# Performance work log

Hardware: AMD Instinct MI355X
Metric: run time of the kernel (lower is better)

Reference implementation:

```python
import jax, jax.numpy as jnp
import numpy as np
from jax import lax

EPS = 1e-5  # BatchNorm eps (inference-style BN with running stats)


def _bn(x, g, b, m, v):
    scale = g / jnp.sqrt(v + EPS)
    return x * scale[None, :, None, None] + (b - m * scale)[None, :, None, None]


def _conv1x1_bn(x, w, g, b, m, v):
    # ConvNormActivation(in_ch, out, k=1, activation=None) -> 1x1 conv (no bias) + BN
    y = jnp.einsum('bchw,oc->bohw', x, w)
    return _bn(y, g, b, m, v)


def _upsample_bilinear_ac(x, scale):
    # nn.Upsample(scale_factor=scale, mode='bilinear', align_corners=True)
    B, C, H, W = x.shape
    Ho, Wo = H * scale, W * scale

    def coords(n_in, n_out):
        s = jnp.arange(n_out, dtype=x.dtype) * ((n_in - 1) / (n_out - 1))
        i0 = jnp.clip(jnp.floor(s).astype(jnp.int32), 0, n_in - 2)
        t = s - i0.astype(x.dtype)
        return i0, t

    iy, ty = coords(H, Ho)
    ix, tx = coords(W, Wo)
    x = x[:, :, iy, :] * (1 - ty)[None, None, :, None] + x[:, :, iy + 1, :] * ty[None, None, :, None]
    x = x[:, :, :, ix] * (1 - tx) + x[:, :, :, ix + 1] * tx
    return x


def _dcnv2(x, off_w, off_b, w):
    # DCNv2: internal 3x3 conv -> 18 offsets (dy,dx per tap) + 9 sigmoid masks,
    # then modulated deformable 3x3 conv (stride 1, pad 1, no bias).
    B, C, H, W = x.shape
    K2 = 9
    om = lax.conv_general_dilated(x, off_w, (1, 1), ((1, 1), (1, 1)),
                                  dimension_numbers=('NCHW', 'OIHW', 'NCHW'))
    om = om + off_b[None, :, None, None]
    off = om[:, :2 * K2].reshape(B, K2, 2, H, W)          # (dy, dx) per kernel tap
    mask = jax.nn.sigmoid(om[:, 2 * K2:3 * K2])           # [B,9,H,W]

    ky, kx = jnp.meshgrid(jnp.arange(3), jnp.arange(3), indexing='ij')
    base_y = (jnp.arange(H)[None, :, None] + (ky.reshape(K2) - 1)[:, None, None]).astype(x.dtype)  # [9,H,1]
    base_x = (jnp.arange(W)[None, None, :] + (kx.reshape(K2) - 1)[:, None, None]).astype(x.dtype)  # [9,1,W]
    sy = base_y[None] + off[:, :, 0]                      # [B,9,H,W]
    sx = base_x[None] + off[:, :, 1]

    xf = x.reshape(B, C, H * W)
    y0 = jnp.floor(sy)
    x0 = jnp.floor(sx)
    val = jnp.zeros((B, C, K2, H, W), x.dtype)
    for dy in (0, 1):
        for dx in (0, 1):
            yy = y0 + dy
            xx = x0 + dx
            wgt = (1 - jnp.abs(sy - yy)) * (1 - jnp.abs(sx - xx))
            valid = (yy >= 0) & (yy <= H - 1) & (xx >= 0) & (xx <= W - 1)
            idx = jnp.clip(yy, 0, H - 1).astype(jnp.int32) * W + jnp.clip(xx, 0, W - 1).astype(jnp.int32)
            g = jnp.take_along_axis(xf, idx.reshape(B, 1, -1), axis=2).reshape(B, C, K2, H, W)
            val = val + g * (wgt * valid.astype(x.dtype))[:, None]
    val = val * mask[:, None]
    return jnp.einsum('bckhw,ock->bohw', val, w.reshape(w.shape[0], C, K2))


def _forward(f0, f1, f2, f3,
             w0, g0, b0, m0, v0, w1, g1, b1, m1, v1,
             w2, g2, b2, m2, v2, w3, g3, b3, m3, v3,
             off_w, off_b, dcn_w, gf, bf, mf, vf):
    x1 = _conv1x1_bn(f0, w0, g0, b0, m0, v0)
    x2 = _upsample_bilinear_ac(_conv1x1_bn(f1, w1, g1, b1, m1, v1), 2)
    x3 = _upsample_bilinear_ac(_conv1x1_bn(f2, w2, g2, b2, m2, v2), 4)
    x4 = _upsample_bilinear_ac(_conv1x1_bn(f3, w3, g3, b3, m3, v3), 8)
    x = jax.nn.relu(x1 + x2 + x3 + x4)
    y = _dcnv2(x, off_w, off_b, dcn_w)
    return jax.nn.relu(_bn(y, gf, bf, mf, vf))


def setup_inputs() -> dict:
    key = jax.random.key(0)
    ks = iter(jax.random.split(key, 64))

    def rn(shape, scale=1.0):
        return jax.random.normal(next(ks), shape, dtype=jnp.float32) * scale

    def ru(shape):
        return jax.random.uniform(next(ks), shape, dtype=jnp.float32)

    C = 64
    inp = {}
    inp['f0'] = rn((4, 64, 160, 160))
    inp['f1'] = rn((4, 128, 80, 80))
    inp['f2'] = rn((4, 256, 40, 40))
    inp['f3'] = rn((4, 512, 20, 20))
    for i, cin in enumerate([64, 128, 256, 512]):
        inp[f'w{i}'] = rn((C, cin), 1.0 / np.sqrt(cin))
        inp[f'g{i}'] = rn((C,))
        inp[f'b{i}'] = rn((C,))
        inp[f'm{i}'] = rn((C,))
        inp[f'v{i}'] = ru((C,))
    inp['off_w'] = rn((27, C, 3, 3), 0.01)   # small offsets, like post-training DCN
    inp['off_b'] = rn((27,), 0.01)
    inp['dcn_w'] = rn((C, C, 3, 3), 1.0 / np.sqrt(C * 9))
    inp['gf'] = rn((C,))
    inp['bf'] = rn((C,))
    inp['mf'] = rn((C,))
    inp['vf'] = ru((C,))
    return inp


def reference(f0, f1, f2, f3,
              w0, g0, b0, m0, v0, w1, g1, b1, m1, v1,
              w2, g2, b2, m2, v2, w3, g3, b3, m3, v3,
              off_w, off_b, dcn_w, gf, bf, mf, vf):
    return _forward(f0, f1, f2, f3,
                    w0, g0, b0, m0, v0, w1, g1, b1, m1, v1,
                    w2, g2, b2, m2, v2, w3, g3, b3, m3, v3,
                    off_w, off_b, dcn_w, gf, bf, mf, vf)
```

## Files before the change

kernel.cpp:

```cpp
#include <hip/hip_runtime.h>
#include <math.h>

#define EPSB 1e-5f

constexpr int B_ = 4;
constexpr int C_ = 64;
constexpr int H_ = 160;
constexpr int W_ = 160;
constexpr int HW_ = H_ * W_;

constexpr size_t X_OFF   = 0;
constexpr size_t Y1_OFF  = X_OFF  + (size_t)B_ * HW_ * 64;
constexpr size_t Y2_OFF  = Y1_OFF + (size_t)B_ * 6400 * 64;
constexpr size_t Y3_OFF  = Y2_OFF + (size_t)B_ * 1600 * 64;
constexpr size_t OM_OFF  = Y3_OFF + (size_t)B_ * 400 * 64;
constexpr size_t WR0_OFF = OM_OFF + (size_t)B_ * HW_ * 27;
constexpr size_t WTB_OFF = WR0_OFF + 4096;
constexpr size_t RWB_OFF = WTB_OFF + (9 * 64 * 72) / 2;
constexpr size_t SB_OFF  = RWB_OFF + (9 * 32 * 64) / 2;
constexpr size_t WR1_OFF = X_OFF + 0;
constexpr size_t WR2_OFF = X_OFF + 8192;
constexpr size_t WR3_OFF = X_OFF + 24576;

typedef short bf16x8 __attribute__((ext_vector_type(8)));
typedef float f32x4 __attribute__((ext_vector_type(4)));
typedef unsigned int u32x2 __attribute__((ext_vector_type(2)));

static __device__ __forceinline__ unsigned short f2bf(float f) {
    unsigned int u = __float_as_uint(f);
    u += 0x7fff + ((u >> 16) & 1);
    return (unsigned short)(u >> 16);
}

__global__ __launch_bounds__(256) void prep_kernel(
    const float* __restrict__ g0, const float* __restrict__ b0, const float* __restrict__ m0, const float* __restrict__ v0,
    const float* __restrict__ g1, const float* __restrict__ b1, const float* __restrict__ m1, const float* __restrict__ v1,
    const float* __restrict__ g2, const float* __restrict__ b2, const float* __restrict__ m2, const float* __restrict__ v2,
    const float* __restrict__ g3, const float* __restrict__ b3, const float* __restrict__ m3, const float* __restrict__ v3,
    const float* __restrict__ gf, const float* __restrict__ bf, const float* __restrict__ mf, const float* __restrict__ vf,
    const float* __restrict__ w0, const float* __restrict__ w1, const float* __restrict__ w2, const float* __restrict__ w3,
    const float* __restrict__ dcn_w, const float* __restrict__ off_w,
    float* __restrict__ ws)
{
    int tid = blockIdx.x * 256 + threadIdx.x;
    if (tid < 320) {
        int j = tid >> 6, c = tid & 63;
        const float *g, *b, *m, *v;
        switch (j) {
            case 0: g = g0; b = b0; m = m0; v = v0; break;
            case 1: g = g1; b = b1; m = m1; v = v1; break;
            case 2: g = g2; b = b2; m = m2; v = v2; break;
            case 3: g = g3; b = b3; m = m3; v = v3; break;
            default: g = gf; b = bf; m = mf; v = vf; break;
        }
        float sc = g[c] * rsqrtf(v[c] + EPSB);
        ws[SB_OFF + j * 128 + c]      = sc;
        ws[SB_OFF + j * 128 + 64 + c] = b[c] - m[c] * sc;
        return;
    }
    int t = tid - 320;
    if (t < 4096) {
        int ci = t >> 6, o = t & 63;
        ws[WR0_OFF + t] = w0[o * 64 + ci];
        return;
    }
    t -= 4096;
    if (t < 9 * 64 * 72) {
        int k = t / 4608, r = t % 4608, o = r / 72, c = r % 72;
        float v = (c < 64) ? dcn_w[o * 576 + c * 9 + k] : 0.f;
        ((unsigned short*)(ws + WTB_OFF))[t] = f2bf(v);
        return;
    }
    t -= 9 * 64 * 72;
    if (t < 9 * 32 * 64) {
        int tap = t >> 11, r = t & 2047, o = r >> 6, ci = r & 63;
        float v = (o < 27) ? off_w[o * 576 + ci * 9 + tap] : 0.f;
        ((unsigned short*)(ws + RWB_OFF))[t] = f2bf(v);
        return;
    }
    t -= 9 * 32 * 64;
    if (t < 8192) {
        int ci = t >> 6, o = t & 63;
        ws[WR1_OFF + t] = w1[o * 128 + ci];
        return;
    }
    t -= 8192;
    if (t < 16384) {
        int ci = t >> 6, o = t & 63;
        ws[WR2_OFF + t] = w2[o * 256 + ci];
        return;
    }
    t -= 16384;
    if (t < 32768) {
        int ci = t >> 6, o = t & 63;
        ws[WR3_OFF + t] = w3[o * 512 + ci];
        return;
    }
}

__global__ __launch_bounds__(256) void conv_all_kernel(
    const float* __restrict__ f1in, const float* __restrict__ f2in, const float* __restrict__ f3in,
    float* __restrict__ ws)
{
    __shared__ float R0[64 * 65];
    __shared__ float R1[64 * 65];
    __shared__ float SBl[128];

    int blk = blockIdx.x;
    const float* fin; const float* wr; const float* sbg; float* yout;
    int Cin, hw, tile;
    if (blk < 400)      { fin = f1in; wr = ws + WR1_OFF; sbg = ws + SB_OFF + 128; yout = ws + Y1_OFF; Cin = 128; hw = 6400; tile = blk; }
    else if (blk < 500) { fin = f2in; wr = ws + WR2_OFF; sbg = ws + SB_OFF + 256; yout = ws + Y2_OFF; Cin = 256; hw = 1600; tile = blk - 400; }
    else                { fin = f3in; wr = ws + WR3_OFF; sbg = ws + SB_OFF + 384; yout = ws + Y3_OFF; Cin = 512; hw = 400;  tile = blk - 500; }

    int tid  = threadIdx.x;
    int lane = tid & 63;
    int wv   = __builtin_amdgcn_readfirstlane(tid >> 6);

    if (tid < 128) SBl[tid] = sbg[tid];

    int P = tile * 64 + lane;
    int b = P / hw;
    int p = P - b * hw;

    int cq = Cin >> 2;
    const float* fb = fin + ((size_t)b * Cin + (size_t)wv * cq) * hw + p;
    const float* wq = wr + (wv * cq) * 64;

    float acc[64];
#pragma unroll
    for (int o = 0; o < 64; o++) acc[o] = 0.f;

    for (int c0 = 0; c0 < cq; c0 += 8) {
        float fv[8];
#pragma unroll
        for (int j = 0; j < 8; j++) fv[j] = fb[(size_t)(c0 + j) * hw];
#pragma unroll
        for (int j = 0; j < 8; j++) {
            const float* wrow = wq + (c0 + j) * 64;
#pragma unroll
            for (int o = 0; o < 64; o++) acc[o] = fmaf(fv[j], wrow[o], acc[o]);
        }
    }

    if (wv == 2) {
#pragma unroll
        for (int o = 0; o < 64; o++) R0[lane * 65 + o] = acc[o];
    }
    if (wv == 3) {
#pragma unroll
        for (int o = 0; o < 64; o++) R1[lane * 65 + o] = acc[o];
    }
    __syncthreads();
    if (wv == 0) {
#pragma unroll
        for (int o = 0; o < 64; o++) acc[o] += R0[lane * 65 + o];
    }
    if (wv == 1) {
#pragma unroll
        for (int o = 0; o < 64; o++) acc[o] += R1[lane * 65 + o];
    }
    __syncthreads();
    if (wv == 1) {
#pragma unroll
        for (int o = 0; o < 64; o++) R0[lane * 65 + o] = acc[o];
    }
    __syncthreads();
    if (wv == 0) {
#pragma unroll
        for (int o = 0; o < 64; o++) {
            float v = acc[o] + R0[lane * 65 + o];
            R1[lane * 65 + o] = fmaf(v, SBl[o], SBl[64 + o]);
        }
    }
    __syncthreads();

#pragma unroll
    for (int it = 0; it < 16; it++) {
        int idx = it * 256 + tid;
        int px = idx >> 6, o = idx & 63;
        yout[(size_t)(tile * 64 + px) * 64 + o] = R1[px * 65 + o];
    }
}

__global__ __launch_bounds__(256) void fuse_kernel(const float* __restrict__ f0, float* __restrict__ ws)
{
    __shared__ float Ot[64 * 68];

    int tid = threadIdx.x;
    int blk = blockIdx.x;
    int xcd = blk & 7, slot = blk >> 3;
    int b = xcd >> 1;
    int t = (xcd & 1) * 200 + slot;
    int p0 = t * 64;
    int lane = tid & 63;
    int cb = __builtin_amdgcn_readfirstlane(tid >> 6);
    int p = p0 + lane;
    const float* wr0 = ws + WR0_OFF + cb * 16;
    const float* sb  = ws + SB_OFF;

    {
        float acc[16];
#pragma unroll
        for (int i = 0; i < 16; i++) acc[i] = 0.f;

        const float* f0b = f0 + (size_t)b * 64 * HW_ + p;
        for (int ci0 = 0; ci0 < 64; ci0 += 16) {
            float fv[16];
#pragma unroll
            for (int j = 0; j < 16; j++) fv[j] = f0b[(size_t)(ci0 + j) * HW_];
#pragma unroll
            for (int j = 0; j < 16; j++) {
                const float* wrow = wr0 + (ci0 + j) * 64;
#pragma unroll
                for (int i = 0; i < 16; i++) acc[i] = fmaf(fv[j], wrow[i], acc[i]);
            }
        }
        float* orow = Ot + lane * 68 + cb * 16;
#pragma unroll
        for (int i = 0; i < 16; i++) {
            int o = cb * 16 + i;
            orow[i] = fmaf(acc[i], sb[o], sb[64 + o]);
        }
    }
    __syncthreads();

    {
        int chunk = lane & 15, pxo = lane >> 4;
        unsigned short* xb = (unsigned short*)(ws + X_OFF) + ((size_t)b * HW_ + p0) * 64;
#pragma unroll
        for (int r = 0; r < 4; r++) {
            int gpx = cb * 16 + r * 4 + pxo;
            int gp = p0 + gpx;
            int h = gp / W_, w = gp % W_;

            float fy1 = h * (79.f / 159.f); int i1 = (int)fy1; if (i1 > 78) i1 = 78; float ty1 = fy1 - i1;
            float fx1 = w * (79.f / 159.f); int j1 = (int)fx1; if (j1 > 78) j1 = 78; float tx1 = fx1 - j1;
            const float* y1 = ws + Y1_OFF + ((size_t)b * 6400 + (size_t)(i1 * 80 + j1)) * 64 + chunk * 4;
            float fy2 = h * (39.f / 159.f); int i2 = (int)fy2; if (i2 > 38) i2 = 38; float ty2 = fy2 - i2;
            float fx2 = w * (39.f / 159.f); int j2 = (int)fx2; if (j2 > 38) j2 = 38; float tx2 = fx2 - j2;
            const float* y2 = ws + Y2_OFF + ((size_t)b * 1600 + (size_t)(i2 * 40 + j2)) * 64 + chunk * 4;
            float fy3 = h * (19.f / 159.f); int i3 = (int)fy3; if (i3 > 18) i3 = 18; float ty3 = fy3 - i3;
            float fx3 = w * (19.f / 159.f); int j3 = (int)fx3; if (j3 > 18) j3 = 18; float tx3 = fx3 - j3;
            const float* y3 = ws + Y3_OFF + ((size_t)b * 400 + (size_t)(i3 * 20 + j3)) * 64 + chunk * 4;

            f32x4 A[12];
            A[0]  = *(const f32x4*)(y1);
            A[1]  = *(const f32x4*)(y1 + 64);
            A[2]  = *(const f32x4*)(y1 + 80 * 64);
            A[3]  = *(const f32x4*)(y1 + 81 * 64);
            A[4]  = *(const f32x4*)(y2);
            A[5]  = *(const f32x4*)(y2 + 64);
            A[6]  = *(const f32x4*)(y2 + 40 * 64);
            A[7]  = *(const f32x4*)(y2 + 41 * 64);
            A[8]  = *(const f32x4*)(y3);
            A[9]  = *(const f32x4*)(y3 + 64);
            A[10] = *(const f32x4*)(y3 + 20 * 64);
            A[11] = *(const f32x4*)(y3 + 21 * 64);

            f32x4 v = *(const f32x4*)(Ot + gpx * 68 + chunk * 4);

            float w00, w01, w10, w11;
            w00 = (1.f - ty1) * (1.f - tx1); w01 = (1.f - ty1) * tx1; w10 = ty1 * (1.f - tx1); w11 = ty1 * tx1;
#pragma unroll
            for (int j = 0; j < 4; j++)
                v[j] += A[0][j] * w00 + A[1][j] * w01 + A[2][j] * w10 + A[3][j] * w11;
            w00 = (1.f - ty2) * (1.f - tx2); w01 = (1.f - ty2) * tx2; w10 = ty2 * (1.f - tx2); w11 = ty2 * tx2;
#pragma unroll
            for (int j = 0; j < 4; j++)
                v[j] += A[4][j] * w00 + A[5][j] * w01 + A[6][j] * w10 + A[7][j] * w11;
            w00 = (1.f - ty3) * (1.f - tx3); w01 = (1.f - ty3) * tx3; w10 = ty3 * (1.f - tx3); w11 = ty3 * tx3;
#pragma unroll
            for (int j = 0; j < 4; j++)
                v[j] += A[8][j] * w00 + A[9][j] * w01 + A[10][j] * w10 + A[11][j] * w11;

#pragma unroll
            for (int j = 0; j < 4; j++) v[j] = fmaxf(v[j], 0.f);
            unsigned int lo = ((unsigned int)f2bf(v[1]) << 16) | f2bf(v[0]);
            unsigned int hi = ((unsigned int)f2bf(v[3]) << 16) | f2bf(v[2]);
            *(u32x2*)(xb + (size_t)gpx * 64 + chunk * 4) = (u32x2){lo, hi};
        }
    }
}

__global__ __launch_bounds__(256, 8) void dcn_fused_kernel(const float* __restrict__ off_b,
                                                           float* __restrict__ ws, float* __restrict__ out)
{
    __shared__ __align__(16) unsigned char SMEM[16640];
    unsigned short* A  = (unsigned short*)SMEM;
    float*          OMs = (float*)(SMEM + 9216);

    int tid = threadIdx.x;
    int blk = blockIdx.x;
    int xcd = blk & 7, slot = blk >> 3;
    int b = xcd >> 1;
    int t = (xcd & 1) * 200 + slot;
    int p0 = t * 64;
    int lane = tid & 63, cb = tid >> 6;
    int px = lane;
    int p = p0 + px;
    int h = p / W_, w = p % W_;
    int mrow = lane & 15, quad = lane >> 4;
    int chunk = lane & 15, pxo = lane >> 4;

    const unsigned short* rwb = (const unsigned short*)(ws + RWB_OFF);
    const unsigned short* wtb = (const unsigned short*)(ws + WTB_OFF);
    const unsigned short* xbh = (const unsigned short*)(ws + X_OFF) + (size_t)b * HW_ * 64;
    const float* sb = ws + SB_OFF + 4 * 128;

    {
        f32x4 acc2[2];
        acc2[0] = (f32x4){0.f, 0.f, 0.f, 0.f};
        acc2[1] = (f32x4){0.f, 0.f, 0.f, 0.f};

        for (int tap = 0; tap < 9; ++tap) {
            int dy = tap / 3 - 1, dx = tap % 3 - 1;
            int delta = dy * W_ + dx;
            int  pss[4];
            bool vlds[4];
#pragma unroll
            for (int r = 0; r < 4; r++) {
                int gpx = cb * 16 + r * 4 + pxo;
                int gp = p0 + gpx;
                int gh = gp / W_, gw = gp % W_;
                int yy = gh + dy, xx = gw + dx;
                vlds[r] = (yy >= 0) && (yy < H_) && (xx >= 0) && (xx < W_);
                int ps = gp + delta;
                pss[r] = min(max(ps, 0), HW_ - 1);
            }
            u32x2 g[4];
#pragma unroll
            for (int r = 0; r < 4; r++)
                g[r] = *(const u32x2*)(xbh + (size_t)pss[r] * 64 + chunk * 4);
#pragma unroll
            for (int r = 0; r < 4; r++) {
                int gpx = cb * 16 + r * 4 + pxo;
                u32x2 gv;
                gv.x = vlds[r] ? g[r].x : 0u;
                gv.y = vlds[r] ? g[r].y : 0u;
                *(u32x2*)(A + gpx * 72 + chunk * 4) = gv;
            }

            const unsigned short* Ab = A + (cb * 16 + mrow) * 72;
#pragma unroll
            for (int ks = 0; ks < 2; ks++) {
                bf16x8 af = *(const bf16x8*)(Ab + ks * 32 + quad * 8);
#pragma unroll
                for (int nt = 0; nt < 2; nt++) {
                    bf16x8 bf_ = *(const bf16x8*)(rwb + tap * 2048 + (nt * 16 + mrow) * 64 + ks * 32 + quad * 8);
                    acc2[nt] = __builtin_amdgcn_mfma_f32_16x16x32_bf16(af, bf_, acc2[nt], 0, 0, 0);
                }
            }
        }

        __syncthreads();
        float* Cl = (float*)SMEM;
#pragma unroll
        for (int nt = 0; nt < 2; nt++) {
            int o = nt * 16 + mrow;
            if (o < 27) {
                int pr = cb * 16 + quad * 4;
#pragma unroll
                for (int r = 0; r < 4; r++) Cl[(pr + r) * 28 + o] = acc2[nt][r];
            }
        }
        __syncthreads();

        for (int k = cb; k < 9; k += 4) {
            float ady = Cl[px * 28 + 2 * k]     + off_b[2 * k];
            float adx = Cl[px * 28 + 2 * k + 1] + off_b[2 * k + 1];
            float am  = Cl[px * 28 + 18 + k]    + off_b[18 + k];
            float sy = (float)(h + k / 3 - 1) + ady;
            float sx = (float)(w + k % 3 - 1) + adx;
            float mk = 1.f / (1.f + __expf(-am));
            OMs[px * 27 + 3 * k]     = sy;
            OMs[px * 27 + 3 * k + 1] = sx;
            OMs[px * 27 + 3 * k + 2] = mk;
        }
        __syncthreads();
    }

    f32x4 acc[4];
#pragma unroll
    for (int nt = 0; nt < 4; nt++) acc[nt] = (f32x4){0.f, 0.f, 0.f, 0.f};

    for (int k = 0; k < 9; ++k) {
#pragma unroll
        for (int rp = 0; rp < 2; rp++) {
            int   idxs[2][4];
            float wvs[2][4];
#pragma unroll
            for (int rr = 0; rr < 2; rr++) {
                int r = rp * 2 + rr;
                int gpx = cb * 16 + r * 4 + pxo;
                float sy = OMs[gpx * 27 + 3 * k];
                float sx = OMs[gpx * 27 + 3 * k + 1];
                float mk = OMs[gpx * 27 + 3 * k + 2];
                float y0f = floorf(sy), x0f = floorf(sx);
                int y0 = (int)y0f, x0 = (int)x0f;
                float ty = sy - y0f, tx = sx - x0f;
#pragma unroll
                for (int cr = 0; cr < 4; cr++) {
                    int dy = cr >> 1, dx = cr & 1;
                    int yy = y0 + dy, xx = x0 + dx;
                    float wy = dy ? ty : 1.f - ty;
                    float wx = dx ? tx : 1.f - tx;
                    bool vld = (yy >= 0) && (yy < H_) && (xx >= 0) && (xx < W_);
                    int yc = min(max(yy, 0), H_ - 1);
                    int xc = min(max(xx, 0), W_ - 1);
                    idxs[rr][cr] = yc * W_ + xc;
                    wvs[rr][cr]  = vld ? wy * wx * mk : 0.f;
                }
            }
            u32x2 g[2][4];
#pragma unroll
            for (int rr = 0; rr < 2; rr++)
#pragma unroll
                for (int cr = 0; cr < 4; cr++)
                    g[rr][cr] = *(const u32x2*)(xbh + (size_t)idxs[rr][cr] * 64 + chunk * 4);
#pragma unroll
            for (int rr = 0; rr < 2; rr++) {
                int r = rp * 2 + rr;
                int gpx = cb * 16 + r * 4 + pxo;
                f32x4 v = (f32x4){0.f, 0.f, 0.f, 0.f};
#pragma unroll
                for (int cr = 0; cr < 4; cr++) {
                    float wv = wvs[rr][cr];
                    float e0 = __uint_as_float(g[rr][cr].x << 16);
                    float e1 = __uint_as_float(g[rr][cr].x & 0xffff0000u);
                    float e2 = __uint_as_float(g[rr][cr].y << 16);
                    float e3 = __uint_as_float(g[rr][cr].y & 0xffff0000u);
                    v[0] = fmaf(e0, wv, v[0]);
                    v[1] = fmaf(e1, wv, v[1]);
                    v[2] = fmaf(e2, wv, v[2]);
                    v[3] = fmaf(e3, wv, v[3]);
                }
                unsigned int lo = ((unsigned int)f2bf(v[1]) << 16) | f2bf(v[0]);
                unsigned int hi = ((unsigned int)f2bf(v[3]) << 16) | f2bf(v[2]);
                *(u32x2*)(A + gpx * 72 + chunk * 4) = (u32x2){lo, hi};
            }
        }

        const unsigned short* Ab = A + (cb * 16 + mrow) * 72;
#pragma unroll
        for (int ks = 0; ks < 2; ks++) {
            bf16x8 af = *(const bf16x8*)(Ab + ks * 32 + quad * 8);
#pragma unroll
            for (int nt = 0; nt < 4; nt++) {
                bf16x8 bf_ = *(const bf16x8*)(wtb + k * 4608 + (nt * 16 + mrow) * 72 + ks * 32 + quad * 8);
                acc[nt] = __builtin_amdgcn_mfma_f32_16x16x32_bf16(af, bf_, acc[nt], 0, 0, 0);
            }
        }
    }

    __syncthreads();
    float* C_lds = (float*)SMEM;
#pragma unroll
    for (int nt = 0; nt < 4; nt++) {
        int o = nt * 16 + mrow;
        int pxb = cb * 16 + quad * 4;
#pragma unroll
        for (int r = 0; r < 4; r++) C_lds[o * 65 + pxb + r] = acc[nt][r];
    }
    __syncthreads();
#pragma unroll
    for (int i = 0; i < 16; i++) {
        int o = cb * 16 + i;
        float v = C_lds[o * 65 + lane];
        v = fmaf(v, sb[o], sb[64 + o]);
        out[((size_t)b * 64 + o) * HW_ + p0 + lane] = fmaxf(v, 0.f);
    }
}

extern "C" void kernel_launch(void* const* d_in, const int* in_sizes, int n_in,
                              void* d_out, int out_size, void* d_ws, size_t ws_size,
                              hipStream_t stream)
{
    const float* f0 = (const float*)d_in[0];
    const float* f1 = (const float*)d_in[1];
    const float* f2 = (const float*)d_in[2];
    const float* f3 = (const float*)d_in[3];
    const float* w0 = (const float*)d_in[4];
    const float* g0 = (const float*)d_in[5];
    const float* b0 = (const float*)d_in[6];
    const float* m0 = (const float*)d_in[7];
    const float* v0 = (const float*)d_in[8];
    const float* w1 = (const float*)d_in[9];
    const float* g1 = (const float*)d_in[10];
    const float* b1 = (const float*)d_in[11];
    const float* m1 = (const float*)d_in[12];
    const float* v1 = (const float*)d_in[13];
    const float* w2 = (const float*)d_in[14];
    const float* g2 = (const float*)d_in[15];
    const float* b2 = (const float*)d_in[16];
    const float* m2 = (const float*)d_in[17];
    const float* v2 = (const float*)d_in[18];
    const float* w3 = (const float*)d_in[19];
    const float* g3 = (const float*)d_in[20];
    const float* b3 = (const float*)d_in[21];
    const float* m3 = (const float*)d_in[22];
    const float* v3 = (const float*)d_in[23];
    const float* off_w = (const float*)d_in[24];
    const float* off_b = (const float*)d_in[25];
    const float* dcn_w = (const float*)d_in[26];
    const float* gf = (const float*)d_in[27];
    const float* bf = (const float*)d_in[28];
    const float* mf = (const float*)d_in[29];
    const float* vf = (const float*)d_in[30];

    float* ws  = (float*)d_ws;
    float* out = (float*)d_out;

    prep_kernel<<<dim3(476), dim3(256), 0, stream>>>(
        g0, b0, m0, v0, g1, b1, m1, v1, g2, b2, m2, v2, g3, b3, m3, v3,
        gf, bf, mf, vf, w0, w1, w2, w3, dcn_w, off_w, ws);

    conv_all_kernel<<<dim3(525), dim3(256), 0, stream>>>(f1, f2, f3, ws);

    fuse_kernel<<<dim3(1600), dim3(256), 0, stream>>>(f0, ws);

    dcn_fused_kernel<<<dim3(1600), dim3(256), 0, stream>>>(off_b, ws, out);
}
```

Measured before the change: 299.6 us.

## Merge low-res and f0 1x1 convs into one launch, split upsample-fuse out

The f0 1x1 conv+BN moves out of the fuse kernel into one combined launch with the f1/f2/f3 1x1 convs. Its result goes to a bf16 workspace buffer so the two kinds of work can share the GPU instead of running back to back. A new fuse2 kernel reads that buffer, adds the three bilinear-upsampled branches, applies ReLU and writes the bf16 input for the DCN. In exchange this adds a global round trip of the intermediate, rounds it to bf16 earlier, and the channel-split reduction now uses a single LDS buffer with extra barriers.

```diff
diff --git a/kernel.cpp b/kernel.cpp
--- a/kernel.cpp
+++ b/kernel.cpp
@@ -21,6 +21,8 @@
 constexpr size_t WR1_OFF = X_OFF + 0;
 constexpr size_t WR2_OFF = X_OFF + 8192;
 constexpr size_t WR3_OFF = X_OFF + 24576;
+constexpr size_t XU_X = 0;
+constexpr size_t XU_O = 6553600;
 
 typedef short bf16x8 __attribute__((ext_vector_type(8)));
 typedef float f32x4 __attribute__((ext_vector_type(4)));
@@ -30,6 +32,9 @@
     unsigned int u = __float_as_uint(f);
     u += 0x7fff + ((u >> 16) & 1);
     return (unsigned short)(u >> 16);
+}
+static __device__ __forceinline__ float bf2f(unsigned short s) {
+    return __uint_as_float((unsigned int)s << 16);
 }
 
 __global__ __launch_bounds__(256) void prep_kernel(
@@ -98,95 +103,140 @@
     }
 }
 
-__global__ __launch_bounds__(256) void conv_all_kernel(
-    const float* __restrict__ f1in, const float* __restrict__ f2in, const float* __restrict__ f3in,
+__global__ __launch_bounds__(256) void produce_kernel(
+    const float* __restrict__ f0in, const float* __restrict__ f1in,
+    const float* __restrict__ f2in, const float* __restrict__ f3in,
     float* __restrict__ ws)
 {
-    __shared__ float R0[64 * 65];
-    __shared__ float R1[64 * 65];
-    __shared__ float SBl[128];
+    __shared__ __align__(16) unsigned char SM[16640];
 
     int blk = blockIdx.x;
-    const float* fin; const float* wr; const float* sbg; float* yout;
-    int Cin, hw, tile;
-    if (blk < 400)      { fin = f1in; wr = ws + WR1_OFF; sbg = ws + SB_OFF + 128; yout = ws + Y1_OFF; Cin = 128; hw = 6400; tile = blk; }
-    else if (blk < 500) { fin = f2in; wr = ws + WR2_OFF; sbg = ws + SB_OFF + 256; yout = ws + Y2_OFF; Cin = 256; hw = 1600; tile = blk - 400; }
-    else                { fin = f3in; wr = ws + WR3_OFF; sbg = ws + SB_OFF + 384; yout = ws + Y3_OFF; Cin = 512; hw = 400;  tile = blk - 500; }
-
     int tid  = threadIdx.x;
     int lane = tid & 63;
-    int wv   = __builtin_amdgcn_readfirstlane(tid >> 6);
-
-    if (tid < 128) SBl[tid] = sbg[tid];
-
-    int P = tile * 64 + lane;
-    int b = P / hw;
-    int p = P - b * hw;
-
-    int cq = Cin >> 2;
-    const float* fb = fin + ((size_t)b * Cin + (size_t)wv * cq) * hw + p;
-    const float* wq = wr + (wv * cq) * 64;
-
-    float acc[64];
-#pragma unroll
-    for (int o = 0; o < 64; o++) acc[o] = 0.f;
-
-    for (int c0 = 0; c0 < cq; c0 += 8) {
-        float fv[8];
-#pragma unroll
-        for (int j = 0; j < 8; j++) fv[j] = fb[(size_t)(c0 + j) * hw];
-#pragma unroll
-        for (int j = 0; j < 8; j++) {
-            const float* wrow = wq + (c0 + j) * 64;
-#pragma unroll
-            for (int o = 0; o < 64; o++) acc[o] = fmaf(fv[j], wrow[o], acc[o]);
-        }
-    }
-
-    if (wv == 2) {
-#pragma unroll
-        for (int o = 0; o < 64; o++) R0[lane * 65 + o] = acc[o];
-    }
-    if (wv == 3) {
-#pragma unroll
-        for (int o = 0; o < 64; o++) R1[lane * 65 + o] = acc[o];
-    }
-    __syncthreads();
-    if (wv == 0) {
-#pragma unroll
-        for (int o = 0; o < 64; o++) acc[o] += R0[lane * 65 + o];
-    }
-    if (wv == 1) {
-#pragma unroll
-        for (int o = 0; o < 64; o++) acc[o] += R1[lane * 65 + o];
-    }
-    __syncthreads();
-    if (wv == 1) {
-#pragma unroll
-        for (int o = 0; o < 64; o++) R0[lane * 65 + o] = acc[o];
-    }
-    __syncthreads();
-    if (wv == 0) {
-#pragma unroll
-        for (int o = 0; o < 64; o++) {
-            float v = acc[o] + R0[lane * 65 + o];
-            R1[lane * 65 + o] = fmaf(v, SBl[o], SBl[64 + o]);
-        }
-    }
-    __syncthreads();
-
-#pragma unroll
-    for (int it = 0; it < 16; it++) {
-        int idx = it * 256 + tid;
-        int px = idx >> 6, o = idx & 63;
-        yout[(size_t)(tile * 64 + px) * 64 + o] = R1[px * 65 + o];
-    }
-}
-
-__global__ __launch_bounds__(256) void fuse_kernel(const float* __restrict__ f0, float* __restrict__ ws)
+
+    if (blk < 525) {
+        float* R0 = (float*)SM;
+        const float* fin; const float* wr; const float* sbg; float* yout;
+        int Cin, hw, tile;
+        if (blk < 400)      { fin = f1in; wr = ws + WR1_OFF; sbg = ws + SB_OFF + 128; yout = ws + Y1_OFF; Cin = 128; hw = 6400; tile = blk; }
+        else if (blk < 500) { fin = f2in; wr = ws + WR2_OFF; sbg = ws + SB_OFF + 256; yout = ws + Y2_OFF; Cin = 256; hw = 1600; tile = blk - 400; }
+        else                { fin = f3in; wr = ws + WR3_OFF; sbg = ws + SB_OFF + 384; yout = ws + Y3_OFF; Cin = 512; hw = 400;  tile = blk - 500; }
+
+        int wv = __builtin_amdgcn_readfirstlane(tid >> 6);
+
+        int P = tile * 64 + lane;
+        int b = P / hw;
+        int p = P - b * hw;
+
+        int cq = Cin >> 2;
+        const float* fb = fin + ((size_t)b * Cin + (size_t)wv * cq) * hw + p;
+        const float* wq = wr + (wv * cq) * 64;
+
+        float acc[64];
+#pragma unroll
+        for (int o = 0; o < 64; o++) acc[o] = 0.f;
+
+        for (int c0 = 0; c0 < cq; c0 += 8) {
+            float fv[8];
+#pragma unroll
+            for (int j = 0; j < 8; j++) fv[j] = fb[(size_t)(c0 + j) * hw];
+#pragma unroll
+            for (int j = 0; j < 8; j++) {
+                const float* wrow = wq + (c0 + j) * 64;
+#pragma unroll
+                for (int o = 0; o < 64; o++) acc[o] = fmaf(fv[j], wrow[o], acc[o]);
+            }
+        }
+
+        if (wv == 2) {
+#pragma unroll
+            for (int o = 0; o < 64; o++) R0[lane * 65 + o] = acc[o];
+        }
+        __syncthreads();
+        if (wv == 0) {
+#pragma unroll
+            for (int o = 0; o < 64; o++) acc[o] += R0[lane * 65 + o];
+        }
+        __syncthreads();
+        if (wv == 3) {
+#pragma unroll
+            for (int o = 0; o < 64; o++) R0[lane * 65 + o] = acc[o];
+        }
+        __syncthreads();
+        if (wv == 1) {
+#pragma unroll
+            for (int o = 0; o < 64; o++) acc[o] += R0[lane * 65 + o];
+        }
+        __syncthreads();
+        if (wv == 1) {
+#pragma unroll
+            for (int o = 0; o < 64; o++) R0[lane * 65 + o] = acc[o];
+        }
+        __syncthreads();
+        if (wv == 0) {
+#pragma unroll
+            for (int o = 0; o < 64; o++) {
+                float v = acc[o] + R0[lane * 65 + o];
+                R0[lane * 65 + o] = fmaf(v, sbg[o], sbg[64 + o]);
+            }
+        }
+        __syncthreads();
+
+#pragma unroll
+        for (int it = 0; it < 16; it++) {
+            int idx = it * 256 + tid;
+            int px = idx >> 6, o = idx & 63;
+            yout[(size_t)(tile * 64 + px) * 64 + o] = R0[px * 65 + o];
+        }
+    } else {
+        unsigned short* Ot = (unsigned short*)SM;
+        int fblk = blk - 525;
+        int xcd = fblk & 7, slot = fblk >> 3;
+        int b = xcd >> 1;
+        int t = (xcd & 1) * 200 + slot;
+        int p0 = t * 64;
+        int cb = __builtin_amdgcn_readfirstlane(tid >> 6);
+        int p = p0 + lane;
+        const float* wr0 = ws + WR0_OFF + cb * 16;
+        const float* sb  = ws + SB_OFF;
+
+        float acc[16];
+#pragma unroll
+        for (int i = 0; i < 16; i++) acc[i] = 0.f;
+
+        const float* f0b = f0in + (size_t)b * 64 * HW_ + p;
+        for (int ci0 = 0; ci0 < 64; ci0 += 8) {
+            float fv[8];
+#pragma unroll
+            for (int j = 0; j < 8; j++) fv[j] = f0b[(size_t)(ci0 + j) * HW_];
+#pragma unroll
+            for (int j = 0; j < 8; j++) {
+                const float* wrow = wr0 + (ci0 + j) * 64;
+#pragma unroll
+                for (int i = 0; i < 16; i++) acc[i] = fmaf(fv[j], wrow[i], acc[i]);
+            }
+        }
+        unsigned short* orow = Ot + lane * 68 + cb * 16;
+#pragma unroll
+        for (int i = 0; i < 16; i++) {
+            int o = cb * 16 + i;
+            orow[i] = f2bf(fmaf(acc[i], sb[o], sb[64 + o]));
+        }
+        __syncthreads();
+
+        unsigned short* Ob = (unsigned short*)ws + XU_O + ((size_t)b * HW_ + p0) * 64;
+#pragma unroll
+        for (int it = 0; it < 8; it++) {
+            int idx = it * 256 + tid;
+            int px = idx >> 5, seg = idx & 31;
+            *(unsigned int*)(Ob + (size_t)px * 64 + seg * 2) =
+                *(const unsigned int*)(Ot + px * 68 + seg * 2);
+        }
+    }
+}
+
+__global__ __launch_bounds__(256) void fuse2_kernel(float* __restrict__ ws)
 {
-    __shared__ float Ot[64 * 68];
-
     int tid = threadIdx.x;
     int blk = blockIdx.x;
     int xcd = blk & 7, slot = blk >> 3;
@@ -195,91 +245,67 @@
     int p0 = t * 64;
     int lane = tid & 63;
     int cb = __builtin_amdgcn_readfirstlane(tid >> 6);
-    int p = p0 + lane;
-    const float* wr0 = ws + WR0_OFF + cb * 16;
-    const float* sb  = ws + SB_OFF;
-
-    {
-        float acc[16];
-#pragma unroll
-        for (int i = 0; i < 16; i++) acc[i] = 0.f;
-
-        const float* f0b = f0 + (size_t)b * 64 * HW_ + p;
-        for (int ci0 = 0; ci0 < 64; ci0 += 16) {
-            float fv[16];
-#pragma unroll
-            for (int j = 0; j < 16; j++) fv[j] = f0b[(size_t)(ci0 + j) * HW_];
-#pragma unroll
-            for (int j = 0; j < 16; j++) {
-                const float* wrow = wr0 + (ci0 + j) * 64;
-#pragma unroll
-                for (int i = 0; i < 16; i++) acc[i] = fmaf(fv[j], wrow[i], acc[i]);
-            }
-        }
-        float* orow = Ot + lane * 68 + cb * 16;
-#pragma unroll
-        for (int i = 0; i < 16; i++) {
-            int o = cb * 16 + i;
-            orow[i] = fmaf(acc[i], sb[o], sb[64 + o]);
-        }
-    }
-    __syncthreads();
-
-    {
-        int chunk = lane & 15, pxo = lane >> 4;
-        unsigned short* xb = (unsigned short*)(ws + X_OFF) + ((size_t)b * HW_ + p0) * 64;
-#pragma unroll
-        for (int r = 0; r < 4; r++) {
-            int gpx = cb * 16 + r * 4 + pxo;
-            int gp = p0 + gpx;
-            int h = gp / W_, w = gp % W_;
-
-            float fy1 = h * (79.f / 159.f); int i1 = (int)fy1; if (i1 > 78) i1 = 78; float ty1 = fy1 - i1;
-            float fx1 = w * (79.f / 159.f); int j1 = (int)fx1; if (j1 > 78) j1 = 78; float tx1 = fx1 - j1;
-            const float* y1 = ws + Y1_OFF + ((size_t)b * 6400 + (size_t)(i1 * 80 + j1)) * 64 + chunk * 4;
-            float fy2 = h * (39.f / 159.f); int i2 = (int)fy2; if (i2 > 38) i2 = 38; float ty2 = fy2 - i2;
-            float fx2 = w * (39.f / 159.f); int j2 = (int)fx2; if (j2 > 38) j2 = 38; float tx2 = fx2 - j2;
-            const float* y2 = ws + Y2_OFF + ((size_t)b * 1600 + (size_t)(i2 * 40 + j2)) * 64 + chunk * 4;
-            float fy3 = h * (19.f / 159.f); int i3 = (int)fy3; if (i3 > 18) i3 = 18; float ty3 = fy3 - i3;
-            float fx3 = w * (19.f / 159.f); int j3 = (int)fx3; if (j3 > 18) j3 = 18; float tx3 = fx3 - j3;
-            const float* y3 = ws + Y3_OFF + ((size_t)b * 400 + (size_t)(i3 * 20 + j3)) * 64 + chunk * 4;
-
-            f32x4 A[12];
-            A[0]  = *(const f32x4*)(y1);
-            A[1]  = *(const f32x4*)(y1 + 64);
-            A[2]  = *(const f32x4*)(y1 + 80 * 64);
-            A[3]  = *(const f32x4*)(y1 + 81 * 64);
-            A[4]  = *(const f32x4*)(y2);
-            A[5]  = *(const f32x4*)(y2 + 64);
-            A[6]  = *(const f32x4*)(y2 + 40 * 64);
-            A[7]  = *(const f32x4*)(y2 + 41 * 64);
-            A[8]  = *(const f32x4*)(y3);
-            A[9]  = *(const f32x4*)(y3 + 64);
-            A[10] = *(const f32x4*)(y3 + 20 * 64);
-            A[11] = *(const f32x4*)(y3 + 21 * 64);
-
-            f32x4 v = *(const f32x4*)(Ot + gpx * 68 + chunk * 4);
-
-            float w00, w01, w10, w11;
-            w00 = (1.f - ty1) * (1.f - tx1); w01 = (1.f - ty1) * tx1; w10 = ty1 * (1.f - tx1); w11 = ty1 * tx1;
-#pragma unroll
-            for (int j = 0; j < 4; j++)
-                v[j] += A[0][j] * w00 + A[1][j] * w01 + A[2][j] * w10 + A[3][j] * w11;
-            w00 = (1.f - ty2) * (1.f - tx2); w01 = (1.f - ty2) * tx2; w10 = ty2 * (1.f - tx2); w11 = ty2 * tx2;
-#pragma unroll
-            for (int j = 0; j < 4; j++)
-                v[j] += A[4][j] * w00 + A[5][j] * w01 + A[6][j] * w10 + A[7][j] * w11;
-            w00 = (1.f - ty3) * (1.f - tx3); w01 = (1.f - ty3) * tx3; w10 = ty3 * (1.f - tx3); w11 = ty3 * tx3;
-#pragma unroll
-            for (int j = 0; j < 4; j++)
-                v[j] += A[8][j] * w00 + A[9][j] * w01 + A[10][j] * w10 + A[11][j] * w11;
-
-#pragma unroll
-            for (int j = 0; j < 4; j++) v[j] = fmaxf(v[j], 0.f);
-            unsigned int lo = ((unsigned int)f2bf(v[1]) << 16) | f2bf(v[0]);
-            unsigned int hi = ((unsigned int)f2bf(v[3]) << 16) | f2bf(v[2]);
-            *(u32x2*)(xb + (size_t)gpx * 64 + chunk * 4) = (u32x2){lo, hi};
-        }
+    int chunk = lane & 15, pxo = lane >> 4;
+
+    const unsigned short* Ob = (const unsigned short*)ws + XU_O + ((size_t)b * HW_ + p0) * 64;
+    unsigned short* xb = (unsigned short*)ws + XU_X + ((size_t)b * HW_ + p0) * 64;
+
+#pragma unroll
+    for (int r = 0; r < 4; r++) {
+        int gpx = cb * 16 + r * 4 + pxo;
+        int gp = p0 + gpx;
+        int h = gp / W_, w = gp % W_;
+
+        float fy1 = h * (79.f / 159.f); int i1 = (int)fy1; if (i1 > 78) i1 = 78; float ty1 = fy1 - i1;
+        float fx1 = w * (79.f / 159.f); int j1 = (int)fx1; if (j1 > 78) j1 = 78; float tx1 = fx1 - j1;
+        const float* y1 = ws + Y1_OFF + ((size_t)b * 6400 + (size_t)(i1 * 80 + j1)) * 64 + chunk * 4;
+        float fy2 = h * (39.f / 159.f); int i2 = (int)fy2; if (i2 > 38) i2 = 38; float ty2 = fy2 - i2;
+        float fx2 = w * (39.f / 159.f); int j2 = (int)fx2; if (j2 > 38) j2 = 38; float tx2 = fx2 - j2;
+        const float* y2 = ws + Y2_OFF + ((size_t)b * 1600 + (size_t)(i2 * 40 + j2)) * 64 + chunk * 4;
+        float fy3 = h * (19.f / 159.f); int i3 = (int)fy3; if (i3 > 18) i3 = 18; float ty3 = fy3 - i3;
+        float fx3 = w * (19.f / 159.f); int j3 = (int)fx3; if (j3 > 18) j3 = 18; float tx3 = fx3 - j3;
+        const float* y3 = ws + Y3_OFF + ((size_t)b * 400 + (size_t)(i3 * 20 + j3)) * 64 + chunk * 4;
+
+        f32x4 A[12];
+        A[0]  = *(const f32x4*)(y1);
+        A[1]  = *(const f32x4*)(y1 + 64);
+        A[2]  = *(const f32x4*)(y1 + 80 * 64);
+        A[3]  = *(const f32x4*)(y1 + 81 * 64);
+        A[4]  = *(const f32x4*)(y2);
+        A[5]  = *(const f32x4*)(y2 + 64);
+        A[6]  = *(const f32x4*)(y2 + 40 * 64);
+        A[7]  = *(const f32x4*)(y2 + 41 * 64);
+        A[8]  = *(const f32x4*)(y3);
+        A[9]  = *(const f32x4*)(y3 + 64);
+        A[10] = *(const f32x4*)(y3 + 20 * 64);
+        A[11] = *(const f32x4*)(y3 + 21 * 64);
+
+        u32x2 ov = *(const u32x2*)(Ob + (size_t)gpx * 64 + chunk * 4);
+        f32x4 v;
+        v[0] = bf2f((unsigned short)(ov.x & 0xffff));
+        v[1] = bf2f((unsigned short)(ov.x >> 16));
+        v[2] = bf2f((unsigned short)(ov.y & 0xffff));
+        v[3] = bf2f((unsigned short)(ov.y >> 16));
+
+        float w00, w01, w10, w11;
+        w00 = (1.f - ty1) * (1.f - tx1); w01 = (1.f - ty1) * tx1; w10 = ty1 * (1.f - tx1); w11 = ty1 * tx1;
+#pragma unroll
+        for (int j = 0; j < 4; j++)
+            v[j] += A[0][j] * w00 + A[1][j] * w01 + A[2][j] * w10 + A[3][j] * w11;
+        w00 = (1.f - ty2) * (1.f - tx2); w01 = (1.f - ty2) * tx2; w10 = ty2 * (1.f - tx2); w11 = ty2 * tx2;
+#pragma unroll
+        for (int j = 0; j < 4; j++)
+            v[j] += A[4][j] * w00 + A[5][j] * w01 + A[6][j] * w10 + A[7][j] * w11;
+        w00 = (1.f - ty3) * (1.f - tx3); w01 = (1.f - ty3) * tx3; w10 = ty3 * (1.f - tx3); w11 = ty3 * tx3;
+#pragma unroll
+        for (int j = 0; j < 4; j++)
+            v[j] += A[8][j] * w00 + A[9][j] * w01 + A[10][j] * w10 + A[11][j] * w11;
+
+#pragma unroll
+        for (int j = 0; j < 4; j++) v[j] = fmaxf(v[j], 0.f);
+        unsigned int lo = ((unsigned int)f2bf(v[1]) << 16) | f2bf(v[0]);
+        unsigned int hi = ((unsigned int)f2bf(v[3]) << 16) | f2bf(v[2]);
+        *(u32x2*)(xb + (size_t)gpx * 64 + chunk * 4) = (u32x2){lo, hi};
     }
 }
 
@@ -305,7 +331,7 @@
 
     const unsigned short* rwb = (const unsigned short*)(ws + RWB_OFF);
     const unsigned short* wtb = (const unsigned short*)(ws + WTB_OFF);
-    const unsigned short* xbh = (const unsigned short*)(ws + X_OFF) + (size_t)b * HW_ * 64;
+    const unsigned short* xbh = (const unsigned short*)ws + XU_X + (size_t)b * HW_ * 64;
     const float* sb = ws + SB_OFF + 4 * 128;
 
     {
@@ -515,9 +541,9 @@
         g0, b0, m0, v0, g1, b1, m1, v1, g2, b2, m2, v2, g3, b3, m3, v3,
         gf, bf, mf, vf, w0, w1, w2, w3, dcn_w, off_w, ws);
 
-    conv_all_kernel<<<dim3(525), dim3(256), 0, stream>>>(f1, f2, f3, ws);
-
-    fuse_kernel<<<dim3(1600), dim3(256), 0, stream>>>(f0, ws);
+    produce_kernel<<<dim3(2125), dim3(256), 0, stream>>>(f0, f1, f2, f3, ws);
+
+    fuse2_kernel<<<dim3(1600), dim3(256), 0, stream>>>(ws);
 
     dcn_fused_kernel<<<dim3(1600), dim3(256), 0, stream>>>(off_b, ws, out);
 }
```

Result: slower. 385.2 us (+28.6%).
